# Kernel tuning notes

Hardware: AMD Instinct MI355X
Metric: run time of the kernel (lower is better)

## Reference

```python
import jax, jax.numpy as jnp
import numpy as np

N_BITS = 4            # W4A4 duquant-style fake quantization
BLOCK = 128           # rotation block size


def _round_ste(x):
    # straight-through rounding (matches round_ste used by LLM quantizers)
    return x + jax.lax.stop_gradient(jnp.round(x) - x)


def _block_rotate(x, R):
    # apply block-diagonal rotation along the last dim: x[..., F] -> x[..., F]
    *lead, F = x.shape
    B = R.shape[0]
    xr = jnp.einsum('...kb,bc->...kc', x.reshape(*lead, F // B, B), R)
    return xr.reshape(*lead, F)


def _fake_quant(x, R, n_bits):
    # rotate -> dynamic asymmetric uniform quant over last dim -> dequant -> de-rotate
    qmax = 2 ** n_bits - 1
    xr = _block_rotate(x, R)
    xmin = jnp.minimum(xr.min(axis=-1, keepdims=True), 0.0)
    xmax = jnp.maximum(xr.max(axis=-1, keepdims=True), 0.0)
    scale = jnp.clip((xmax - xmin) / qmax, 1e-5, None)
    zero_point = jax.lax.stop_gradient(jnp.round(-xmin / scale))
    xq = jnp.clip(_round_ste(xr / scale) + zero_point, 0.0, float(qmax))
    xdq = (xq - zero_point) * scale
    return _block_rotate(xdq, R.T)


def setup_inputs() -> dict:
    key = jax.random.key(0)
    k1, k2, k3 = jax.random.split(key, 3)
    x = jax.random.normal(k1, (4, 2048, 4096), dtype=jnp.float32)
    weight = jax.random.normal(k2, (4096, 4096), dtype=jnp.float32) * 0.02
    bias = jax.random.normal(k3, (4096,), dtype=jnp.float32) * 0.01
    # fixed orthogonal rotation matrix (DuQuant learned/constructed rotation)
    rng = np.random.default_rng(0)
    Rnp, _ = np.linalg.qr(rng.standard_normal((BLOCK, BLOCK)).astype(np.float32))
    R = jnp.asarray(Rnp, dtype=jnp.float32)
    return {"input": x, "weight": weight, "bias": bias, "R": R}


def reference(input, weight, bias, R):
    # act fake-quant (use_act_quant=True), weight fake-quant (use_weight_quant=True)
    x_q = _fake_quant(input, R, N_BITS)        # [B, S, Fin]
    w_q = _fake_quant(weight, R, N_BITS)       # [Fout, Fin], per-out-channel quant
    out = jnp.einsum('bsi,oi->bso', x_q, w_q) + bias
    return out
```

## Files before the change

kernel.cpp:

```cpp
#include <hip/hip_runtime.h>
#include <hip/hip_bf16.h>
#include <stdint.h>


typedef __bf16    bf16x8 __attribute__((ext_vector_type(8)));
typedef float     f32x4  __attribute__((ext_vector_type(4)));
typedef int       i32x4  __attribute__((ext_vector_type(4)));
typedef uint32_t  u32;
typedef uint32_t  u32x4  __attribute__((ext_vector_type(4)));

__device__ __forceinline__ void gload_lds16(const void* g, void* l) {
  __builtin_amdgcn_global_load_lds(
      (__attribute__((address_space(1))) void*)(g),
      (__attribute__((address_space(3))) void*)(l), 16, 0, 0);
}

__global__ __launch_bounds__(256)
void prep_rt(const float* __restrict__ R, unsigned short* __restrict__ RT3)
{
  const int tid = blockIdx.x * 256 + threadIdx.x;
  const int q  = tid & 7;
  const int l  = (tid >> 3) & 63;
  const int f  = (tid >> 9) & 7;
  const int ks = tid >> 12;
  const float v = R[(ks * 32 + (l >> 4) * 8 + q) * 128 + f * 16 + (l & 15)];
  __hip_bfloat16 h1 = __float2bfloat16(v);
  const float rem = v - __bfloat162float(h1);
  __hip_bfloat16 h2 = __float2bfloat16(rem);
  const float rem2 = rem - __bfloat162float(h2);
  __hip_bfloat16 h3 = __float2bfloat16(rem2);
  RT3[tid]          = *(unsigned short*)&h1;
  RT3[16384 + tid]  = *(unsigned short*)&h2;
  RT3[32768 + tid]  = *(unsigned short*)&h3;
}

#define FQ_TB  98304
#define FQ_SC  (98304 + 8 * 2560)

__global__ __launch_bounds__(512, 2)
void fq_rot1p(const float* __restrict__ X,
              const unsigned short* __restrict__ RT3,
              uint8_t* __restrict__ Q,
              float4* __restrict__ stats)
{
  __shared__ __align__(16) char lds[98304 + 8 * 2560 + 1664];

  const int t = threadIdx.x, lane = t & 63, wid = t >> 6;
  const size_t rowbase = (size_t)blockIdx.x * 16;
  const int colw = wid * 512;

#pragma unroll
  for (int i = 0; i < 12; ++i)
    gload_lds16((const char*)RT3 + i * 8192 + t * 16, lds + i * 8192 + t * 16);
  asm volatile("s_waitcnt vmcnt(0)" ::: "memory");
  __syncthreads();

  float* smin  = (float*)(lds + FQ_SC);
  float* smax  = (float*)(lds + FQ_SC + 512);
  float* rowsc = (float*)(lds + FQ_SC + 1024);
  float* rowzp = (float*)(lds + FQ_SC + 1088);
  int*   qsumL = (int*)  (lds + FQ_SC + 1152);

  const float* xbase = X + (rowbase + (lane & 15)) * 4096 + colw + (lane >> 4) * 8;

  f32x4 acc[4][8];
#pragma unroll
  for (int b = 0; b < 4; ++b)
#pragma unroll
    for (int f = 0; f < 8; ++f) acc[b][f] = (f32x4){0.f, 0.f, 0.f, 0.f};

#pragma unroll 1
  for (int kk = 0; kk < 4; ++kk) {
    union { bf16x8 v; unsigned short u[8]; } xh[4], xl[4], x2[4];
#pragma unroll
    for (int b = 0; b < 4; ++b) {
      const f32x4 lo = *(const f32x4*)(xbase + b * 128 + kk * 32);
      const f32x4 hi = *(const f32x4*)(xbase + b * 128 + kk * 32 + 4);
#pragma unroll
      for (int e = 0; e < 8; ++e) {
        const float xv = (e < 4) ? lo[e] : hi[e - 4];
        __hip_bfloat16 h1 = __float2bfloat16(xv);
        const float rm = xv - __bfloat162float(h1);
        __hip_bfloat16 h2 = __float2bfloat16(rm);
        const float rm2 = rm - __bfloat162float(h2);
        __hip_bfloat16 h3 = __float2bfloat16(rm2);
        xh[b].u[e] = *(unsigned short*)&h1;
        xl[b].u[e] = *(unsigned short*)&h2;
        x2[b].u[e] = *(unsigned short*)&h3;
      }
    }
#pragma unroll
    for (int f = 0; f < 8; ++f) {
      const int off = ((kk * 8 + f) * 64 + lane) * 16;
      const bf16x8 bh = *(const bf16x8*)(lds + off);
      const bf16x8 bl = *(const bf16x8*)(lds + 32768 + off);
      const bf16x8 b2 = *(const bf16x8*)(lds + 65536 + off);
#pragma unroll
      for (int b = 0; b < 4; ++b)
        acc[b][f] = __builtin_amdgcn_mfma_f32_16x16x32_bf16(bh, xh[b].v, acc[b][f], 0, 0, 0);
#pragma unroll
      for (int b = 0; b < 4; ++b)
        acc[b][f] = __builtin_amdgcn_mfma_f32_16x16x32_bf16(bh, xl[b].v, acc[b][f], 0, 0, 0);
#pragma unroll
      for (int b = 0; b < 4; ++b)
        acc[b][f] = __builtin_amdgcn_mfma_f32_16x16x32_bf16(bh, x2[b].v, acc[b][f], 0, 0, 0);
#pragma unroll
      for (int b = 0; b < 4; ++b)
        acc[b][f] = __builtin_amdgcn_mfma_f32_16x16x32_bf16(bl, xh[b].v, acc[b][f], 0, 0, 0);
#pragma unroll
      for (int b = 0; b < 4; ++b)
        acc[b][f] = __builtin_amdgcn_mfma_f32_16x16x32_bf16(bl, xl[b].v, acc[b][f], 0, 0, 0);
#pragma unroll
      for (int b = 0; b < 4; ++b)
        acc[b][f] = __builtin_amdgcn_mfma_f32_16x16x32_bf16(b2, xh[b].v, acc[b][f], 0, 0, 0);
    }
  }

  float mn = 0.f, mx = 0.f;
#pragma unroll
  for (int b = 0; b < 4; ++b)
#pragma unroll
    for (int f = 0; f < 8; ++f)
#pragma unroll
      for (int r = 0; r < 4; ++r) {
        mn = fminf(mn, acc[b][f][r]);
        mx = fmaxf(mx, acc[b][f][r]);
      }
  mn = fminf(mn, __shfl_xor(mn, 16, 64));
  mn = fminf(mn, __shfl_xor(mn, 32, 64));
  mx = fmaxf(mx, __shfl_xor(mx, 16, 64));
  mx = fmaxf(mx, __shfl_xor(mx, 32, 64));
  if (lane < 16) { smin[wid * 16 + lane] = mn; smax[wid * 16 + lane] = mx; }
  __syncthreads();
  if (t < 16) {
    float m = 0.f, M = 0.f;
#pragma unroll
    for (int q = 0; q < 8; ++q) {
      m = fminf(m, smin[q * 16 + t]);
      M = fmaxf(M, smax[q * 16 + t]);
    }
    const float sc = fmaxf((M - m) / 15.0f, 1e-5f);
    rowsc[t] = sc;
    rowzp[t] = rintf(-m / sc);
  }
  __syncthreads();
  const float scale = rowsc[lane & 15];
  const float zp    = rowzp[lane & 15];

  u32* tw = (u32*)(lds + FQ_TB + wid * 2560);
  int qsum = 0;
#pragma unroll
  for (int b = 0; b < 4; ++b) {
#pragma unroll
    for (int f = 0; f < 8; ++f) {
      u32 pk = 0;
#pragma unroll
      for (int r = 0; r < 4; ++r) {
        const float qf = fminf(fmaxf(rintf(acc[b][f][r] / scale) + zp, 0.0f), 15.0f);
        const int qi = (int)qf;
        qsum += qi;
        pk |= (u32)qi << (8 * r);
      }
      tw[(lane & 15) * 40 + f * 4 + (lane >> 4)] = pk;
    }
#pragma unroll
    for (int rr = 0; rr < 2; ++rr) {
      const int row = rr * 8 + (lane >> 3);
      const int ch  = lane & 7;
      const u32x4 v = *(const u32x4*)&tw[row * 40 + ch * 4];
      *(u32x4*)(Q + (rowbase + row) * 4096 + colw + b * 128 + ch * 16) = v;
    }
  }

  qsum += __shfl_xor(qsum, 16, 64);
  qsum += __shfl_xor(qsum, 32, 64);
  if (lane < 16) qsumL[wid * 16 + lane] = qsum;
  __syncthreads();
  if (t < 16) {
    int S = 0;
#pragma unroll
    for (int q = 0; q < 8; ++q) S += qsumL[q * 16 + t];
    stats[rowbase + t] = make_float4(rowsc[t], rowzp[t], (float)S, 0.0f);
  }
}

__global__ __launch_bounds__(256)
void prep_cols(const float4* __restrict__ Wst, float* __restrict__ colS,
               float* __restrict__ colA, float* __restrict__ colB)
{
  const int n = blockIdx.x * 256 + threadIdx.x;
  const float4 w = Wst[n];
  colS[n] = w.x;
  colA[n] = w.x * w.z - 4096.0f * w.x * w.y;
  colB[n] = w.x * w.y;
}

#define NT 32

__global__ __launch_bounds__(512, 2)
void gemm256_8ph_i8(const uint8_t* __restrict__ Ap,
                    const uint8_t* __restrict__ Bp,
                    const float4* __restrict__ Xst,
                    const float* __restrict__ colS,
                    const float* __restrict__ colA,
                    const float* __restrict__ colB,
                    const float* __restrict__ bias,
                    float* __restrict__ C)
{
  __shared__ __align__(16) uint8_t lds[131072];
  char* ldsB = (char*)lds;
  const char* ldsc = (const char*)lds;

  const int tid  = threadIdx.x;
  const int lane = tid & 63;
  const int wid  = tid >> 6;
  const int wm   = wid >> 2;
  const int wn   = wid & 3;

  int bid = blockIdx.x;
  int nwg = gridDim.x;
  int swz = ((nwg & 7) == 0) ? ((bid & 7) * (nwg >> 3) + (bid >> 3)) : bid;
  const int bm = (swz >> 4) * 256;
  const int bn = (swz & 15) * 256;

  const int t16 = tid * 16;
  int stOff0, stOff1;
  {
    int Lb0 = t16;
    int Lb1 = t16 + 8192;
    int Lp0 = Lb0 ^ (((Lb0 >> 9) & 1) << 5);
    int Lp1 = Lb1 ^ (((Lb1 >> 9) & 1) << 5);
    int s0 = Lp0 >> 10, w0 = Lp0 & 1023;
    int s1 = Lp1 >> 10, w1 = Lp1 & 1023;
    int r0 = ((s0 >> 1) << 4) | (w0 >> 6);
    int k0 = ((s0 & 1) << 6) | (w0 & 63);
    int r1 = ((s1 >> 1) << 4) | (w1 >> 6);
    int k1 = ((s1 & 1) << 6) | (w1 & 63);
    stOff0 = r0 * 4096 + k0;
    stOff1 = r1 * 4096 + k1;
  }

  int swzw = (lane & 15) * 64 + (lane >> 4) * 16;
  swzw ^= ((swzw & 512) ? 32 : 0);

#define STAGE(GP, GROW, KT, SLOT) do {                                   \
    const uint8_t* _g = (GP) + ((size_t)(GROW)) * 4096 + (KT);           \
    gload_lds16(_g + stOff0, ldsB + (SLOT) + t16);                       \
    gload_lds16(_g + stOff1, ldsB + (SLOT) + 8192 + t16);                \
  } while (0)

  i32x4 acc[8][4];
#pragma unroll
  for (int i = 0; i < 8; ++i)
#pragma unroll
    for (int j = 0; j < 4; ++j) acc[i][j] = (i32x4){0, 0, 0, 0};

  STAGE(Bp, bn,       0, 32768);
  STAGE(Ap, bm,       0, 0);
  STAGE(Ap, bm + 128, 0, 16384);
  STAGE(Bp, bn + 128, 0, 49152);
  STAGE(Bp, bn,       128, 65536 + 32768);
  STAGE(Ap, bm,       128, 65536);
  STAGE(Ap, bm + 128, 128, 65536 + 16384);
  asm volatile("s_waitcnt vmcnt(6)" ::: "memory");
  __builtin_amdgcn_s_barrier();

  const int wmOff = wm * 16384;
  const int wnOff = (wn >> 1) * 16384 + (wn & 1) * 8192;

#define LDA(P, I, KK) (*(const i32x4*)((P) + ((I) * 2 + (KK)) * 1024))
#define LDB(P, J, KK) (*(const i32x4*)((P) + ((J) * 2 + (KK)) * 1024))

#define MF16(I0, A00, A01, I1, A10, A11)                                      \
  acc[I0][0] = __builtin_amdgcn_mfma_i32_16x16x64_i8(A00, b00, acc[I0][0], 0, 0, 0); \
  acc[I0][1] = __builtin_amdgcn_mfma_i32_16x16x64_i8(A00, b10, acc[I0][1], 0, 0, 0); \
  acc[I0][2] = __builtin_amdgcn_mfma_i32_16x16x64_i8(A00, b20, acc[I0][2], 0, 0, 0); \
  acc[I0][3] = __builtin_amdgcn_mfma_i32_16x16x64_i8(A00, b30, acc[I0][3], 0, 0, 0); \
  acc[I1][0] = __builtin_amdgcn_mfma_i32_16x16x64_i8(A10, b00, acc[I1][0], 0, 0, 0); \
  acc[I1][1] = __builtin_amdgcn_mfma_i32_16x16x64_i8(A10, b10, acc[I1][1], 0, 0, 0); \
  acc[I1][2] = __builtin_amdgcn_mfma_i32_16x16x64_i8(A10, b20, acc[I1][2], 0, 0, 0); \
  acc[I1][3] = __builtin_amdgcn_mfma_i32_16x16x64_i8(A10, b30, acc[I1][3], 0, 0, 0); \
  acc[I0][0] = __builtin_amdgcn_mfma_i32_16x16x64_i8(A01, b01, acc[I0][0], 0, 0, 0); \
  acc[I0][1] = __builtin_amdgcn_mfma_i32_16x16x64_i8(A01, b11, acc[I0][1], 0, 0, 0); \
  acc[I0][2] = __builtin_amdgcn_mfma_i32_16x16x64_i8(A01, b21, acc[I0][2], 0, 0, 0); \
  acc[I0][3] = __builtin_amdgcn_mfma_i32_16x16x64_i8(A01, b31, acc[I0][3], 0, 0, 0); \
  acc[I1][0] = __builtin_amdgcn_mfma_i32_16x16x64_i8(A11, b01, acc[I1][0], 0, 0, 0); \
  acc[I1][1] = __builtin_amdgcn_mfma_i32_16x16x64_i8(A11, b11, acc[I1][1], 0, 0, 0); \
  acc[I1][2] = __builtin_amdgcn_mfma_i32_16x16x64_i8(A11, b21, acc[I1][2], 0, 0, 0); \
  acc[I1][3] = __builtin_amdgcn_mfma_i32_16x16x64_i8(A11, b31, acc[I1][3], 0, 0, 0);

#define TILE(T, D) do {                                                       \
    const char* aP = ldsc + (D) * 65536 + wmOff + swzw;                       \
    const char* bP = ldsc + (D) * 65536 + 32768 + wnOff + swzw;               \
               \
    i32x4 b00 = LDB(bP, 0, 0), b01 = LDB(bP, 0, 1);                           \
    i32x4 b10 = LDB(bP, 1, 0), b11 = LDB(bP, 1, 1);                           \
    i32x4 b20 = LDB(bP, 2, 0), b21 = LDB(bP, 2, 1);                           \
    i32x4 b30 = LDB(bP, 3, 0), b31 = LDB(bP, 3, 1);                           \
    i32x4 a00 = LDA(aP, 0, 0), a01 = LDA(aP, 0, 1);                           \
    i32x4 a10 = LDA(aP, 1, 0), a11 = LDA(aP, 1, 1);                           \
    if ((T) + 1 < NT) STAGE(Bp, bn + 128, ((T) + 1) * 128, ((D) ^ 1) * 65536 + 49152); \
    __builtin_amdgcn_s_barrier();                                             \
    asm volatile("s_waitcnt lgkmcnt(0)" ::: "memory");                        \
    __builtin_amdgcn_s_setprio(1);                                            \
    MF16(0, a00, a01, 1, a10, a11);                                           \
    __builtin_amdgcn_s_setprio(0);                                            \
    __builtin_amdgcn_sched_barrier(0);                                        \
                                        \
    i32x4 a20 = LDA(aP, 2, 0), a21 = LDA(aP, 2, 1);                           \
    i32x4 a30 = LDA(aP, 3, 0), a31 = LDA(aP, 3, 1);                           \
    i32x4 a40 = LDA(aP, 4, 0), a41 = LDA(aP, 4, 1);                           \
    i32x4 a50 = LDA(aP, 5, 0), a51 = LDA(aP, 5, 1);                           \
    i32x4 a60 = LDA(aP, 6, 0), a61 = LDA(aP, 6, 1);                           \
    i32x4 a70 = LDA(aP, 7, 0), a71 = LDA(aP, 7, 1);                           \
    __builtin_amdgcn_s_barrier();                                             \
    asm volatile("s_waitcnt lgkmcnt(0)" ::: "memory");                        \
    __builtin_amdgcn_s_setprio(1);                                            \
    MF16(2, a20, a21, 3, a30, a31);                                           \
    __builtin_amdgcn_s_setprio(0);                                            \
    __builtin_amdgcn_sched_barrier(0);                                        \
                                       \
    if ((T) + 2 < NT) STAGE(Bp, bn, ((T) + 2) * 128, (D) * 65536 + 32768);    \
    __builtin_amdgcn_s_barrier();                                             \
    __builtin_amdgcn_s_setprio(1);                                            \
    MF16(4, a40, a41, 5, a50, a51);                                           \
    __builtin_amdgcn_s_setprio(0);                                            \
    __builtin_amdgcn_sched_barrier(0);                                        \
                                    \
    if ((T) + 2 < NT) {                                                       \
      STAGE(Ap, bm,       ((T) + 2) * 128, (D) * 65536);                      \
      STAGE(Ap, bm + 128, ((T) + 2) * 128, (D) * 65536 + 16384);              \
    }                                                                         \
    __builtin_amdgcn_s_barrier();                                             \
    __builtin_amdgcn_s_setprio(1);                                            \
    MF16(6, a60, a61, 7, a70, a71);                                           \
    __builtin_amdgcn_s_setprio(0);                                            \
    if ((T) + 2 < NT)      { asm volatile("s_waitcnt vmcnt(6)" ::: "memory"); } \
    else if ((T) + 1 < NT) { asm volatile("s_waitcnt vmcnt(0)" ::: "memory"); } \
    __builtin_amdgcn_sched_barrier(0);                                        \
        \
    __builtin_amdgcn_s_barrier();                                             \
  } while (0)

  for (int t = 0; t < NT; t += 2) {
    TILE(t, 0);
    TILE(t + 1, 1);
  }

  {
    float* tile = (float*)ldsB;
    const int P = 268;
#pragma unroll 1
    for (int quarter = 0; quarter < 4; ++quarter) {
      __builtin_amdgcn_s_barrier();
      if (wm == (quarter >> 1)) {
        const int qi0 = (quarter & 1) * 4;
#pragma unroll
        for (int i = 0; i < 4; ++i)
#pragma unroll
          for (int j = 0; j < 4; ++j) {
            const int rl = i * 16 + (lane >> 4) * 4;
            const int cl = wn * 64 + j * 16 + (lane & 15);
#pragma unroll
            for (int r = 0; r < 4; ++r)
              tile[(rl + r) * P + cl] = (float)acc[qi0 + i][j][r];
          }
      }
      __builtin_amdgcn_s_barrier();
#pragma unroll 1
      for (int rr = 0; rr < 8; ++rr) {
        const int rl = wid * 8 + rr;
        const int grow = bm + quarter * 64 + rl;
        const float4 xs4 = Xst[grow];
        const float r1 = xs4.x, r2 = xs4.x * xs4.y, r3 = xs4.x * xs4.z;
        const int n0 = bn + lane * 4;
        const f32x4 v  = *(const f32x4*)&tile[rl * P + lane * 4];
        const f32x4 cs = *(const f32x4*)&colS[n0];
        const f32x4 ca = *(const f32x4*)&colA[n0];
        const f32x4 cb = *(const f32x4*)&colB[n0];
        const f32x4 bi = *(const f32x4*)&bias[n0];
        f32x4 o;
#pragma unroll
        for (int e = 0; e < 4; ++e)
          o[e] = r1 * cs[e] * v[e] - r2 * ca[e] - r3 * cb[e] + bi[e];
        __builtin_nontemporal_store(o, (f32x4*)&C[(size_t)grow * 4096 + n0]);
      }
    }
  }
#undef TILE
#undef MF16
#undef LDA
#undef LDB
#undef STAGE
}

extern "C" void kernel_launch(void* const* d_in, const int* in_sizes, int n_in,
                              void* d_out, int out_size, void* d_ws, size_t ws_size,
                              hipStream_t stream)
{
  const float* x    = (const float*)d_in[0];
  const float* wgt  = (const float*)d_in[1];
  const float* bias = (const float*)d_in[2];
  const float* R    = (const float*)d_in[3];

  const int K = 4096, N = 4096;
  const int M = in_sizes[0] / K;

  uint8_t* Qx = (uint8_t*)d_ws;
  uint8_t* Qw = Qx + (size_t)M * K;
  float4*  Sx = (float4*)(Qw + (size_t)N * K);
  float4*  Sw = Sx + M;
  unsigned short* RT3 = (unsigned short*)(Sw + N);
  float* colS = (float*)((char*)RT3 + 98304);
  float* colA = colS + N;
  float* colB = colA + N;

  prep_rt<<<64, 256, 0, stream>>>(R, RT3);
  fq_rot1p<<<M / 16, 512, 0, stream>>>(x,   RT3, Qx, Sx);
  fq_rot1p<<<N / 16, 512, 0, stream>>>(wgt, RT3, Qw, Sw);
  prep_cols<<<N / 256, 256, 0, stream>>>(Sw, colS, colA, colB);

  const int nblk = (M / 256) * (N / 256);
  gemm256_8ph_i8<<<nblk, 512, 0, stream>>>(Qx, Qw, Sx, colS, colA, colB, bias,
                                           (float*)d_out);
}
```

Baseline: 288.3 us.

## Split 256x256 int8 GEMM tile across 16 waves with direct epilogue stores

```diff
diff --git a/kernel.cpp b/kernel.cpp
--- a/kernel.cpp
+++ b/kernel.cpp
@@ -197,8 +197,8 @@
 
 #define NT 32
 
-__global__ __launch_bounds__(512, 2)
-void gemm256_8ph_i8(const uint8_t* __restrict__ Ap,
+__global__ __launch_bounds__(1024, 4)
+void gemm256_16w_i8(const uint8_t* __restrict__ Ap,
                     const uint8_t* __restrict__ Bp,
                     const float4* __restrict__ Xst,
                     const float* __restrict__ colS,
@@ -224,34 +224,23 @@
   const int bn = (swz & 15) * 256;
 
   const int t16 = tid * 16;
-  int stOff0, stOff1;
+  int stOff;
   {
-    int Lb0 = t16;
-    int Lb1 = t16 + 8192;
-    int Lp0 = Lb0 ^ (((Lb0 >> 9) & 1) << 5);
-    int Lp1 = Lb1 ^ (((Lb1 >> 9) & 1) << 5);
-    int s0 = Lp0 >> 10, w0 = Lp0 & 1023;
-    int s1 = Lp1 >> 10, w1 = Lp1 & 1023;
-    int r0 = ((s0 >> 1) << 4) | (w0 >> 6);
-    int k0 = ((s0 & 1) << 6) | (w0 & 63);
-    int r1 = ((s1 >> 1) << 4) | (w1 >> 6);
-    int k1 = ((s1 & 1) << 6) | (w1 & 63);
-    stOff0 = r0 * 4096 + k0;
-    stOff1 = r1 * 4096 + k1;
+    int Lp = t16 ^ (((t16 >> 9) & 1) << 5);
+    int s = Lp >> 10, w = Lp & 1023;
+    stOff = ((((s >> 1) << 4) | (w >> 6)) * 4096) + (((s & 1) << 6) | (w & 63));
   }
 
   int swzw = (lane & 15) * 64 + (lane >> 4) * 16;
   swzw ^= ((swzw & 512) ? 32 : 0);
 
-#define STAGE(GP, GROW, KT, SLOT) do {                                   \
-    const uint8_t* _g = (GP) + ((size_t)(GROW)) * 4096 + (KT);           \
-    gload_lds16(_g + stOff0, ldsB + (SLOT) + t16);                       \
-    gload_lds16(_g + stOff1, ldsB + (SLOT) + 8192 + t16);                \
-  } while (0)
-
-  i32x4 acc[8][4];
-#pragma unroll
-  for (int i = 0; i < 8; ++i)
+#define STAGE(GP, GROW, KT, SLOT)                                        \
+    gload_lds16((GP) + ((size_t)(GROW)) * 4096 + (KT) + stOff,           \
+                ldsB + (SLOT) + t16)
+
+  i32x4 acc[4][4];
+#pragma unroll
+  for (int i = 0; i < 4; ++i)
 #pragma unroll
     for (int j = 0; j < 4; ++j) acc[i][j] = (i32x4){0, 0, 0, 0};
 
@@ -260,16 +249,13 @@
   STAGE(Ap, bm + 128, 0, 16384);
   STAGE(Bp, bn + 128, 0, 49152);
   STAGE(Bp, bn,       128, 65536 + 32768);
-  STAGE(Ap, bm,       128, 65536);
-  STAGE(Ap, bm + 128, 128, 65536 + 16384);
-  asm volatile("s_waitcnt vmcnt(6)" ::: "memory");
+  asm volatile("s_waitcnt vmcnt(1)" ::: "memory");
   __builtin_amdgcn_s_barrier();
 
-  const int wmOff = wm * 16384;
-  const int wnOff = (wn >> 1) * 16384 + (wn & 1) * 8192;
-
-#define LDA(P, I, KK) (*(const i32x4*)((P) + ((I) * 2 + (KK)) * 1024))
-#define LDB(P, J, KK) (*(const i32x4*)((P) + ((J) * 2 + (KK)) * 1024))
+  const int aOff = (wm >> 1) * 16384 + (wm & 1) * 8192;
+  const int bOff = 32768 + (wn >> 1) * 16384 + (wn & 1) * 8192;
+
+#define LDF(P, I, KK) (*(const i32x4*)((P) + ((I) * 2 + (KK)) * 1024))
 
 #define MF16(I0, A00, A01, I1, A10, A11)                                      \
   acc[I0][0] = __builtin_amdgcn_mfma_i32_16x16x64_i8(A00, b00, acc[I0][0], 0, 0, 0); \
@@ -290,52 +276,36 @@
   acc[I1][3] = __builtin_amdgcn_mfma_i32_16x16x64_i8(A11, b31, acc[I1][3], 0, 0, 0);
 
 #define TILE(T, D) do {                                                       \
-    const char* aP = ldsc + (D) * 65536 + wmOff + swzw;                       \
-    const char* bP = ldsc + (D) * 65536 + 32768 + wnOff + swzw;               \
-               \
-    i32x4 b00 = LDB(bP, 0, 0), b01 = LDB(bP, 0, 1);                           \
-    i32x4 b10 = LDB(bP, 1, 0), b11 = LDB(bP, 1, 1);                           \
-    i32x4 b20 = LDB(bP, 2, 0), b21 = LDB(bP, 2, 1);                           \
-    i32x4 b30 = LDB(bP, 3, 0), b31 = LDB(bP, 3, 1);                           \
-    i32x4 a00 = LDA(aP, 0, 0), a01 = LDA(aP, 0, 1);                           \
-    i32x4 a10 = LDA(aP, 1, 0), a11 = LDA(aP, 1, 1);                           \
-    if ((T) + 1 < NT) STAGE(Bp, bn + 128, ((T) + 1) * 128, ((D) ^ 1) * 65536 + 49152); \
+    const char* aP = ldsc + (D) * 65536 + aOff + swzw;                        \
+    const char* bP = ldsc + (D) * 65536 + bOff + swzw;                        \
+     \
+    i32x4 b00 = LDF(bP, 0, 0), b01 = LDF(bP, 0, 1);                           \
+    i32x4 b10 = LDF(bP, 1, 0), b11 = LDF(bP, 1, 1);                           \
+    i32x4 b20 = LDF(bP, 2, 0), b21 = LDF(bP, 2, 1);                           \
+    i32x4 b30 = LDF(bP, 3, 0), b31 = LDF(bP, 3, 1);                           \
+    i32x4 a00 = LDF(aP, 0, 0), a01 = LDF(aP, 0, 1);                           \
+    i32x4 a10 = LDF(aP, 1, 0), a11 = LDF(aP, 1, 1);                           \
+    if ((T) + 1 < NT) {                                                       \
+      STAGE(Bp, bn + 128, ((T) + 1) * 128, ((D) ^ 1) * 65536 + 49152);        \
+      STAGE(Ap, bm,       ((T) + 1) * 128, ((D) ^ 1) * 65536);                \
+      STAGE(Ap, bm + 128, ((T) + 1) * 128, ((D) ^ 1) * 65536 + 16384);        \
+    }                                                                         \
     __builtin_amdgcn_s_barrier();                                             \
     asm volatile("s_waitcnt lgkmcnt(0)" ::: "memory");                        \
     __builtin_amdgcn_s_setprio(1);                                            \
     MF16(0, a00, a01, 1, a10, a11);                                           \
     __builtin_amdgcn_s_setprio(0);                                            \
     __builtin_amdgcn_sched_barrier(0);                                        \
-                                        \
-    i32x4 a20 = LDA(aP, 2, 0), a21 = LDA(aP, 2, 1);                           \
-    i32x4 a30 = LDA(aP, 3, 0), a31 = LDA(aP, 3, 1);                           \
-    i32x4 a40 = LDA(aP, 4, 0), a41 = LDA(aP, 4, 1);                           \
-    i32x4 a50 = LDA(aP, 5, 0), a51 = LDA(aP, 5, 1);                           \
-    i32x4 a60 = LDA(aP, 6, 0), a61 = LDA(aP, 6, 1);                           \
-    i32x4 a70 = LDA(aP, 7, 0), a71 = LDA(aP, 7, 1);                           \
+        \
+    i32x4 a20 = LDF(aP, 2, 0), a21 = LDF(aP, 2, 1);                           \
+    i32x4 a30 = LDF(aP, 3, 0), a31 = LDF(aP, 3, 1);                           \
     __builtin_amdgcn_s_barrier();                                             \
     asm volatile("s_waitcnt lgkmcnt(0)" ::: "memory");                        \
+    if ((T) + 2 < NT) STAGE(Bp, bn, ((T) + 2) * 128, (D) * 65536 + 32768);    \
     __builtin_amdgcn_s_setprio(1);                                            \
     MF16(2, a20, a21, 3, a30, a31);                                           \
     __builtin_amdgcn_s_setprio(0);                                            \
-    __builtin_amdgcn_sched_barrier(0);                                        \
-                                       \
-    if ((T) + 2 < NT) STAGE(Bp, bn, ((T) + 2) * 128, (D) * 65536 + 32768);    \
-    __builtin_amdgcn_s_barrier();                                             \
-    __builtin_amdgcn_s_setprio(1);                                            \
-    MF16(4, a40, a41, 5, a50, a51);                                           \
-    __builtin_amdgcn_s_setprio(0);                                            \
-    __builtin_amdgcn_sched_barrier(0);                                        \
-                                    \
-    if ((T) + 2 < NT) {                                                       \
-      STAGE(Ap, bm,       ((T) + 2) * 128, (D) * 65536);                      \
-      STAGE(Ap, bm + 128, ((T) + 2) * 128, (D) * 65536 + 16384);              \
-    }                                                                         \
-    __builtin_amdgcn_s_barrier();                                             \
-    __builtin_amdgcn_s_setprio(1);                                            \
-    MF16(6, a60, a61, 7, a70, a71);                                           \
-    __builtin_amdgcn_s_setprio(0);                                            \
-    if ((T) + 2 < NT)      { asm volatile("s_waitcnt vmcnt(6)" ::: "memory"); } \
+    if ((T) + 2 < NT)      { asm volatile("s_waitcnt vmcnt(1)" ::: "memory"); } \
     else if ((T) + 1 < NT) { asm volatile("s_waitcnt vmcnt(0)" ::: "memory"); } \
     __builtin_amdgcn_sched_barrier(0);                                        \
         \
@@ -347,50 +317,26 @@
     TILE(t + 1, 1);
   }
 
-  {
-    float* tile = (float*)ldsB;
-    const int P = 268;
-#pragma unroll 1
-    for (int quarter = 0; quarter < 4; ++quarter) {
-      __builtin_amdgcn_s_barrier();
-      if (wm == (quarter >> 1)) {
-        const int qi0 = (quarter & 1) * 4;
-#pragma unroll
-        for (int i = 0; i < 4; ++i)
-#pragma unroll
-          for (int j = 0; j < 4; ++j) {
-            const int rl = i * 16 + (lane >> 4) * 4;
-            const int cl = wn * 64 + j * 16 + (lane & 15);
-#pragma unroll
-            for (int r = 0; r < 4; ++r)
-              tile[(rl + r) * P + cl] = (float)acc[qi0 + i][j][r];
-          }
-      }
-      __builtin_amdgcn_s_barrier();
-#pragma unroll 1
-      for (int rr = 0; rr < 8; ++rr) {
-        const int rl = wid * 8 + rr;
-        const int grow = bm + quarter * 64 + rl;
-        const float4 xs4 = Xst[grow];
-        const float r1 = xs4.x, r2 = xs4.x * xs4.y, r3 = xs4.x * xs4.z;
-        const int n0 = bn + lane * 4;
-        const f32x4 v  = *(const f32x4*)&tile[rl * P + lane * 4];
-        const f32x4 cs = *(const f32x4*)&colS[n0];
-        const f32x4 ca = *(const f32x4*)&colA[n0];
-        const f32x4 cb = *(const f32x4*)&colB[n0];
-        const f32x4 bi = *(const f32x4*)&bias[n0];
-        f32x4 o;
-#pragma unroll
-        for (int e = 0; e < 4; ++e)
-          o[e] = r1 * cs[e] * v[e] - r2 * ca[e] - r3 * cb[e] + bi[e];
-        __builtin_nontemporal_store(o, (f32x4*)&C[(size_t)grow * 4096 + n0]);
+#pragma unroll
+  for (int j = 0; j < 4; ++j) {
+    const int n = bn + wn * 64 + j * 16 + (lane & 15);
+    const float cs = colS[n], ca = colA[n], cb = colB[n], bv = bias[n];
+#pragma unroll
+    for (int i = 0; i < 4; ++i) {
+      const int m0 = bm + wm * 64 + i * 16 + (lane >> 4) * 4;
+#pragma unroll
+      for (int r = 0; r < 4; ++r) {
+        const float4 xst = Xst[m0 + r];
+        const float d = (float)acc[i][j][r];
+        const float o = xst.x * cs * d - (xst.x * xst.y) * ca
+                        - (xst.x * xst.z) * cb + bv;
+        __builtin_nontemporal_store(o, &C[(size_t)(m0 + r) * 4096 + n]);
       }
     }
   }
 #undef TILE
 #undef MF16
-#undef LDA
-#undef LDB
+#undef LDF
 #undef STAGE
 }
 
@@ -421,6 +367,6 @@
   prep_cols<<<N / 256, 256, 0, stream>>>(Sw, colS, colA, colB);
 
   const int nblk = (M / 256) * (N / 256);
-  gemm256_8ph_i8<<<nblk, 512, 0, stream>>>(Qx, Qw, Sx, colS, colA, colB, bias,
-                                           (float*)d_out);
-}
+  gemm256_16w_i8<<<nblk, 1024, 0, stream>>>(Qx, Qw, Sx, colS, colA, colB, bias,
+                                            (float*)d_out);
+}
```

Result: slower. 452.6 us (+57.0%).
